# Kernel optimization log

Hardware: AMD Instinct MI355X
Metric: run time of the kernel (lower is better)

The kernel has to match this reference:

```python
import jax, jax.numpy as jnp
import numpy as np

V, E, Hdim, T, B = 32000, 1024, 1024, 64, 32

def setup_inputs() -> dict:
    key = jax.random.key(0)
    ks = jax.random.split(key, 8)
    return {
        "input_x": jax.random.randint(ks[0], (B, T), 0, V, dtype=jnp.int64),
        "initial_state": jnp.zeros((B, Hdim), dtype=jnp.float32),
        "emb": jax.random.normal(ks[1], (V, E), dtype=jnp.float32) * 0.02,
        "H": jax.random.normal(ks[2], (Hdim, Hdim), dtype=jnp.float32) * 0.02,
        "I": jax.random.normal(ks[3], (E, Hdim), dtype=jnp.float32) * 0.02,
        "b1": jax.random.normal(ks[4], (1, Hdim), dtype=jnp.float32) * 0.02,
        "U": jax.random.normal(ks[5], (Hdim, V), dtype=jnp.float32) * 0.02,
        "b2": jax.random.normal(ks[6], (1, V), dtype=jnp.float32) * 0.02,
    }

def reference(input_x, initial_state, emb, H, I, b1, U, b2):
    # Embedding lookup: [B,T] -> [T,B,E] (scan over time)
    x = emb[input_x]                      # [B,T,E]
    x = jnp.transpose(x, (1, 0, 2))       # [T,B,E]

    def step(h, x_t):
        h = jax.nn.sigmoid(h @ H + x_t @ I + b1)  # Elman cell
        return h, h

    final_state, hs = jax.lax.scan(step, initial_state, x)  # hs: [T,B,Hdim]
    # Projection to vocab logits (dropout is identity at eval / p=0)
    logits = jnp.einsum('tbh,hv->tbv', hs, U) + b2          # [T,B,V]
    return logits, final_state
```

## Files before the change

kernel.cpp:

```cpp
#include <hip/hip_runtime.h>


typedef _Float16 f16;
typedef f16 f16x4 __attribute__((ext_vector_type(4)));
typedef f16 f16x8 __attribute__((ext_vector_type(8)));
typedef float f32x4 __attribute__((ext_vector_type(4)));

static constexpr int Vv = 32000, Ee = 1024, Hd = 1024, Tt = 64, Bb = 32;
static constexpr int Mm = Tt * Bb;
static constexpr int NBR = 64;
static constexpr int NBT = 192;

#define GLOAD16(g, l)                                                          \
  __builtin_amdgcn_global_load_lds(                                            \
      (const __attribute__((address_space(1))) void*)(g),                      \
      (__attribute__((address_space(3))) void*)(l), 16, 0, 0)

__global__ __launch_bounds__(256) void prep_all(
    const float* __restrict__ Im, f16* __restrict__ It,
    const float* __restrict__ Hm, f16* __restrict__ Ht,
    const int* __restrict__ tok, const float* __restrict__ emb,
    f16* __restrict__ xg,
    const float* __restrict__ h0, f16* __restrict__ h0f) {
  __shared__ float t[32][33];
  const int tid = threadIdx.x;
  const int bid = blockIdx.x;

  if (bid < 2048) {
    const float* in = (bid < 1024) ? Im : Hm;
    f16* out = (bid < 1024) ? It : Ht;
    const int tile = bid & 1023;
    const int n0 = (tile & 31) * 32, k0 = (tile >> 5) * 32;
    const int tx = tid & 31, ty = tid >> 5;
#pragma unroll
    for (int i = 0; i < 32; i += 8)
      t[ty + i][tx] = in[(size_t)(k0 + ty + i) * 1024 + n0 + tx];
    __syncthreads();
#pragma unroll
    for (int i = 0; i < 32; i += 8)
      out[(size_t)(n0 + ty + i) * 1024 + k0 + tx] = (f16)t[tx][ty + i];
  } else if (bid < 4096) {
    const int m = bid - 2048;
    const int b = m % Bb, tt2 = m / Bb;
    const int token = tok[b * Tt + tt2];
    const float* src = emb + (size_t)token * Ee;
    f16* dst = xg + (size_t)m * Ee;
    const int e = tid * 4;
    float4 v = *(const float4*)(src + e);
    f16x4 o = {(f16)v.x, (f16)v.y, (f16)v.z, (f16)v.w};
    *(f16x4*)(dst + e) = o;
  } else {
    const int i = (bid - 4096) * 256 + tid;
    h0f[i] = (f16)h0[i];
  }
}

__global__ __launch_bounds__(256) void gemm_f16(
    const f16* __restrict__ A, const f16* __restrict__ Bt,
    const float* __restrict__ bias, float* __restrict__ C, int M, int N, int K) {
  __shared__ __align__(16) f16 As[128 * 64];
  __shared__ __align__(16) f16 Bs[128 * 64];

  const int nwg = gridDim.x, bid = blockIdx.x;
  const int cpx = nwg >> 3;
  const int i = (bid & 7) * cpx + (bid >> 3);
  const int ntm = M >> 7;
  const int tm = i % ntm, tn = i / ntm;

  const int tid = threadIdx.x;
  const int lane = tid & 63, wid = tid >> 6;
  const int wm = wid >> 1, wn = wid & 1;

  const int srow = lane >> 3;
  const int sslot = (lane & 7) ^ srow;
  const f16* gA = A + (size_t)(tm * 128 + wid * 8 + srow) * K + sslot * 8;
  const f16* gB = Bt + (size_t)(tn * 128 + wid * 8 + srow) * K + sslot * 8;
  f16* lA = As + wid * 512;
  f16* lB = Bs + wid * 512;

  f32x4 acc[4][4] = {};
  const int r = lane & 15, kb = lane >> 4;

  for (int kc = 0; kc < K; kc += 64) {
    __syncthreads();
#pragma unroll
    for (int rr = 0; rr < 4; ++rr) {
      GLOAD16(gA + (size_t)rr * 32 * K + kc, lA + rr * 2048);
      GLOAD16(gB + (size_t)rr * 32 * K + kc, lB + rr * 2048);
    }
    __syncthreads();

#pragma unroll
    for (int kk = 0; kk < 2; ++kk) {
      f16x8 af[4], bf[4];
#pragma unroll
      for (int ii = 0; ii < 4; ++ii) {
        const int rowA = wm * 64 + ii * 16 + r;
        const int rowB = wn * 64 + ii * 16 + r;
        const int slot = ((kk * 4 + kb) ^ (r & 7)) * 8;
        af[ii] = *(const f16x8*)(As + rowA * 64 + slot);
        bf[ii] = *(const f16x8*)(Bs + rowB * 64 + slot);
      }
#pragma unroll
      for (int ii = 0; ii < 4; ++ii)
#pragma unroll
        for (int jj = 0; jj < 4; ++jj)
          acc[ii][jj] = __builtin_amdgcn_mfma_f32_16x16x32_f16(af[ii], bf[jj], acc[ii][jj], 0, 0, 0);
    }
  }

  const int col0 = tn * 128 + wn * 64, row0 = tm * 128 + wm * 64;
#pragma unroll
  for (int ii = 0; ii < 4; ++ii)
#pragma unroll
    for (int jj = 0; jj < 4; ++jj) {
      int c = col0 + jj * 16 + (lane & 15);
      int rbase = row0 + ii * 16 + (lane >> 4) * 4;
      float bv = bias ? bias[c] : 0.f;
#pragma unroll
      for (int rr = 0; rr < 4; ++rr)
        C[(size_t)(rbase + rr) * N + c] = acc[ii][jj][rr] + bv;
    }
}

#define BAR __builtin_amdgcn_s_barrier()
#define LG0 asm volatile("s_waitcnt lgkmcnt(0)")

__global__ __launch_bounds__(512) void gemm256(
    const f16* __restrict__ A, const f16* __restrict__ Bt,
    const float* __restrict__ bias, float* __restrict__ C,
    int M, int N, int K) {
  __shared__ __align__(16) f16 sm[65536];

  const int nwg = gridDim.x, bid = blockIdx.x;
  const int cpx = nwg >> 3;
  const int ii = (bid & 7) * cpx + (bid >> 3);
  const int ntm = M >> 8;
  const int tm = ii % ntm, tn = ii / ntm;

  const int tid = threadIdx.x;
  const int lane = tid & 63, w = tid >> 6;
  const int wm = w >> 2, wn = w & 3;
  const int r = lane & 15, kb = lane >> 4;

  const int srow = tid >> 3;
  const int slot8 = ((tid & 7) ^ (srow & 7)) * 8;
  const f16* gA = A + (size_t)(tm * 256 + srow) * K + slot8;
  const f16* gB = Bt + (size_t)(tn * 256 + srow) * K + slot8;
  const int lw = w * 512;

  const int NK = K >> 6;

  f32x4 acc[8][4] = {};
  f16x8 a[4][2], b[4][2];

#define STG(kt, ab, R0)                                                        \
  do {                                                                         \
    const f16* gsrc = (ab) ? gB : gA;                                          \
    f16* lb = sm + ((kt) & 1) * 32768 + (ab) * 16384 + (R0) * 64 + lw;         \
    GLOAD16(gsrc + (size_t)(R0) * K + (kt) * 64, lb);                          \
    GLOAD16(gsrc + (size_t)((R0) + 64) * K + (kt) * 64, lb + 4096);            \
  } while (0)

#define LDA(MH)                                                                \
  _Pragma("unroll") for (int i = 0; i < 4; ++i)                                \
  _Pragma("unroll") for (int kk = 0; kk < 2; ++kk)                             \
      a[i][kk] = *(const f16x8*)(Abuf + (wm * 128 + (MH) * 64 + i * 16 + r) * 64 + \
                                 (((kk * 4 + kb) ^ (r & 7)) * 8));

#define LDB(J0)                                                                \
  _Pragma("unroll") for (int j = 0; j < 2; ++j)                                \
  _Pragma("unroll") for (int kk = 0; kk < 2; ++kk)                             \
      b[(J0) + j][kk] = *(const f16x8*)(Bbuf + (wn * 64 + ((J0) + j) * 16 + r) * 64 + \
                                        (((kk * 4 + kb) ^ (r & 7)) * 8));

#define MFMA_Q(MI0, J0)                                                        \
  __builtin_amdgcn_s_setprio(1);                                               \
  _Pragma("unroll") for (int mi = 0; mi < 4; ++mi)                             \
  _Pragma("unroll") for (int j = 0; j < 2; ++j)                                \
  _Pragma("unroll") for (int kk = 0; kk < 2; ++kk)                             \
      acc[(MI0) + mi][(J0) + j] = __builtin_amdgcn_mfma_f32_16x16x32_f16(      \
          a[mi][kk], b[(J0) + j][kk], acc[(MI0) + mi][(J0) + j], 0, 0, 0);     \
  __builtin_amdgcn_s_setprio(0);

  STG(0, 0, 0); STG(0, 0, 128);
  STG(0, 1, 0); STG(0, 1, 128);
  STG(1, 0, 0); STG(1, 0, 128);
  asm volatile("s_waitcnt vmcnt(4)");
  BAR;

  for (int k = 0; k < NK; ++k) {
    const f16* Abuf = sm + (k & 1) * 32768;
    const f16* Bbuf = Abuf + 16384;
    const int kn1 = (k + 1 == NK) ? 0 : k + 1;
    const int kn2 = (k + 2 >= NK) ? k + 2 - NK : k + 2;

    LDA(0); LDB(0);
    STG(kn1, 1, 0);
    BAR; LG0;
    MFMA_Q(0, 0);
    BAR;

    LDB(2);
    STG(kn1, 1, 128);
    BAR; LG0;
    MFMA_Q(0, 2);
    BAR;

    LDA(1);
    BAR; LG0;
    MFMA_Q(4, 2);
    BAR;

    STG(kn2, 0, 0); STG(kn2, 0, 128);
    BAR;
    MFMA_Q(4, 0);
    asm volatile("s_waitcnt vmcnt(4)");
    BAR;
  }

#pragma unroll
  for (int mi = 0; mi < 8; ++mi)
#pragma unroll
    for (int j = 0; j < 4; ++j) {
      int c = tn * 256 + wn * 64 + j * 16 + r;
      int rbase = tm * 256 + wm * 128 + mi * 16 + kb * 4;
      float bv = bias[c];
#pragma unroll
      for (int q = 0; q < 4; ++q)
        __builtin_nontemporal_store(acc[mi][j][q] + bv,
                                    C + (size_t)(rbase + q) * N + c);
    }
#undef STG
#undef LDA
#undef LDB
#undef MFMA_Q
}

__global__ __launch_bounds__(256) void rec_plus_transpose(
    const f16* __restrict__ Ht,
    const float* __restrict__ xI,
    const f16* __restrict__ h0f,
    f16* __restrict__ hs,
    float* __restrict__ hN,
    int* __restrict__ cnt,
    const float* __restrict__ Um,
    f16* __restrict__ Ut) {
  __shared__ float red[4][512];
  __shared__ float tt[32][33];
  const int tid = threadIdx.x;

  if (blockIdx.x >= NBR) {
    const int tb = blockIdx.x - NBR;
    const int tx = tid & 31, ty = tid >> 5;
    const int ntile_n = Vv / 32;
    const int ntiles = ntile_n * (Hd / 32);
    for (int tile = tb; tile < ntiles; tile += NBT) {
      const int n0 = (tile % ntile_n) * 32, k0 = (tile / ntile_n) * 32;
#pragma unroll
      for (int i = 0; i < 32; i += 8)
        tt[ty + i][tx] =
            __builtin_nontemporal_load(Um + (size_t)(k0 + ty + i) * Vv + n0 + tx);
      __syncthreads();
#pragma unroll
      for (int i = 0; i < 32; i += 8)
        Ut[(size_t)(n0 + ty + i) * Hd + k0 + tx] = (f16)tt[tx][ty + i];
      __syncthreads();
      __builtin_amdgcn_s_sleep(16);
    }
    return;
  }

  const int lane = tid & 63, w = tid >> 6;
  const int bn = blockIdx.x;
  const int r = lane & 15, kb = lane >> 4;
  const int colg = bn * 16 + r;

  f16x8 bH[8];
#pragma unroll
  for (int ks = 0; ks < 8; ++ks)
    bH[ks] = *(const f16x8*)(Ht + (size_t)colg * Hd + w * 256 + ks * 32 + kb * 8);

  const int eb = tid >> 3, ecp = tid & 7;

  for (int t = 0; t < Tt; ++t) {
    const f16* hp = t ? hs + (size_t)(t - 1) * Bb * Hd : h0f;
    const float2 xv = *(const float2*)(xI + (size_t)(t * Bb + eb) * Hd + bn * 16 + 2 * ecp);
    f32x4 acc[2] = {};
#pragma unroll
    for (int mt = 0; mt < 2; ++mt) {
      f16x8 af[8];
#pragma unroll
      for (int ks = 0; ks < 8; ++ks)
        af[ks] = *(const f16x8*)(hp + (size_t)(mt * 16 + r) * Hd + w * 256 + ks * 32 + kb * 8);
#pragma unroll
      for (int ks = 0; ks < 8; ++ks)
        acc[mt] = __builtin_amdgcn_mfma_f32_16x16x32_f16(af[ks], bH[ks], acc[mt], 0, 0, 0);
    }
#pragma unroll
    for (int mt = 0; mt < 2; ++mt)
#pragma unroll
      for (int q = 0; q < 4; ++q)
        red[w][mt * 256 + (kb * 4 + q) * 16 + r] = acc[mt][q];
    __syncthreads();

    {
      const float2 r0 = *(const float2*)&red[0][eb * 16 + 2 * ecp];
      const float2 r1 = *(const float2*)&red[1][eb * 16 + 2 * ecp];
      const float2 r2 = *(const float2*)&red[2][eb * 16 + 2 * ecp];
      const float2 r3 = *(const float2*)&red[3][eb * 16 + 2 * ecp];
      float v0 = r0.x + r1.x + r2.x + r3.x + xv.x;
      float v1 = r0.y + r1.y + r2.y + r3.y + xv.y;
      float s0 = 1.f / (1.f + __expf(-v0));
      float s1 = 1.f / (1.f + __expf(-v1));
      union { f16 h[2]; unsigned u; } pk;
      pk.h[0] = (f16)s0;
      pk.h[1] = (f16)s1;
      unsigned* dst = (unsigned*)(hs + (size_t)(t * Bb + eb) * Hd + bn * 16 + 2 * ecp);
      __hip_atomic_store(dst, pk.u, __ATOMIC_RELAXED, __HIP_MEMORY_SCOPE_AGENT);
      if (t == Tt - 1)
        *(float2*)(hN + (size_t)eb * Hd + bn * 16 + 2 * ecp) = make_float2(s0, s1);
    }

    __syncthreads();
    if (tid == 0)
      (void)__hip_atomic_fetch_add(cnt, 1, __ATOMIC_RELAXED, __HIP_MEMORY_SCOPE_AGENT);
    const int target = (t + 1) * NBR;
    while (__hip_atomic_load(cnt, __ATOMIC_RELAXED, __HIP_MEMORY_SCOPE_AGENT) < target)
      __builtin_amdgcn_s_sleep(1);
    asm volatile("" ::: "memory");
  }
}

extern "C" void kernel_launch(void* const* d_in, const int* in_sizes, int n_in,
                              void* d_out, int out_size, void* d_ws, size_t ws_size,
                              hipStream_t stream) {
  const int* input_x = (const int*)d_in[0];
  const float* h0 = (const float*)d_in[1];
  const float* emb = (const float*)d_in[2];
  const float* Hm = (const float*)d_in[3];
  const float* Im = (const float*)d_in[4];
  const float* b1 = (const float*)d_in[5];
  const float* Um = (const float*)d_in[6];
  const float* b2 = (const float*)d_in[7];
  float* out = (float*)d_out;

  char* ws = (char*)d_ws;
  size_t off = 0;
  auto alloc = [&](size_t bytes) { void* p = ws + off; off = (off + bytes + 255) & ~(size_t)255; return p; };
  f16* Ut = (f16*)alloc((size_t)Vv * Hd * 2);
  f16* It = (f16*)alloc((size_t)Hd * Ee * 2);
  f16* Ht = (f16*)alloc((size_t)Hd * Hd * 2);
  f16* xg = (f16*)alloc((size_t)Mm * Ee * 2);
  float* xI = (float*)alloc((size_t)Mm * Hd * 4);
  f16* hs = (f16*)alloc((size_t)Mm * Hd * 2);
  f16* h0f = (f16*)alloc((size_t)Bb * Hd * 2);
  int* cnt = (int*)alloc(256);
  (void)ws_size; (void)in_sizes; (void)n_in; (void)out_size;

  hipMemsetAsync(cnt, 0, sizeof(int), stream);

  prep_all<<<4224, 256, 0, stream>>>(Im, It, Hm, Ht, input_x, emb, xg, h0, h0f);

  gemm_f16<<<(Mm / 128) * (Hd / 128), 256, 0, stream>>>(xg, It, b1, xI, Mm, Hd, Ee);

  rec_plus_transpose<<<NBR + NBT, 256, 0, stream>>>(
      Ht, xI, h0f, hs, out + (size_t)Mm * Vv, cnt, Um, Ut);

  gemm256<<<(Mm / 256) * (Vv / 256), 512, 0, stream>>>(hs, Ut, b2, out, Mm, Vv, Hd);
}
```

Baseline: 459.7 us.

## Fuse recurrence with vocab projection via persistent workers gated on timestep counter

```diff
diff --git a/kernel.cpp b/kernel.cpp
--- a/kernel.cpp
+++ b/kernel.cpp
@@ -9,7 +9,8 @@
 static constexpr int Vv = 32000, Ee = 1024, Hd = 1024, Tt = 64, Bb = 32;
 static constexpr int Mm = Tt * Bb;
 static constexpr int NBR = 64;
-static constexpr int NBT = 192;
+static constexpr int NBW = 192;
+static constexpr int NTM = Mm / 256, NTN = Vv / 256;
 
 #define GLOAD16(g, l)                                                          \
   __builtin_amdgcn_global_load_lds(                                            \
@@ -55,6 +56,20 @@
   }
 }
 
+__global__ void transpose_cvt(const float* __restrict__ in, f16* __restrict__ out,
+                              int K, int N) {
+  __shared__ float t[32][33];
+  int n0 = blockIdx.x * 32, k0 = blockIdx.y * 32;
+  int tx = threadIdx.x, ty = threadIdx.y;
+#pragma unroll
+  for (int i = 0; i < 32; i += 8)
+    t[ty + i][tx] = in[(size_t)(k0 + ty + i) * N + n0 + tx];
+  __syncthreads();
+#pragma unroll
+  for (int i = 0; i < 32; i += 8)
+    out[(size_t)(n0 + ty + i) * K + k0 + tx] = (f16)t[tx][ty + i];
+}
+
 __global__ __launch_bounds__(256) void gemm_f16(
     const f16* __restrict__ A, const f16* __restrict__ Bt,
     const float* __restrict__ bias, float* __restrict__ C, int M, int N, int K) {
@@ -126,40 +141,111 @@
 #define BAR __builtin_amdgcn_s_barrier()
 #define LG0 asm volatile("s_waitcnt lgkmcnt(0)")
 
-__global__ __launch_bounds__(512) void gemm256(
-    const f16* __restrict__ A, const f16* __restrict__ Bt,
-    const float* __restrict__ bias, float* __restrict__ C,
-    int M, int N, int K) {
+__global__ __launch_bounds__(512) void rec_proj(
+    const f16* __restrict__ Ht,
+    const float* __restrict__ xI,
+    const f16* __restrict__ h0f,
+    f16* __restrict__ hs,
+    float* __restrict__ hN,
+    int* __restrict__ cnt,
+    const f16* __restrict__ Ut,
+    const float* __restrict__ b2,
+    float* __restrict__ out) {
   __shared__ __align__(16) f16 sm[65536];
-
-  const int nwg = gridDim.x, bid = blockIdx.x;
-  const int cpx = nwg >> 3;
-  const int ii = (bid & 7) * cpx + (bid >> 3);
-  const int ntm = M >> 8;
-  const int tm = ii % ntm, tn = ii / ntm;
-
   const int tid = threadIdx.x;
-  const int lane = tid & 63, w = tid >> 6;
-  const int wm = w >> 2, wn = w & 3;
-  const int r = lane & 15, kb = lane >> 4;
-
-  const int srow = tid >> 3;
-  const int slot8 = ((tid & 7) ^ (srow & 7)) * 8;
-  const f16* gA = A + (size_t)(tm * 256 + srow) * K + slot8;
-  const f16* gB = Bt + (size_t)(tn * 256 + srow) * K + slot8;
-  const int lw = w * 512;
-
-  const int NK = K >> 6;
-
-  f32x4 acc[8][4] = {};
-  f16x8 a[4][2], b[4][2];
+  const int bid = blockIdx.x;
+
+  if (bid < NBR) {
+    float(*red)[512] = (float(*)[512])sm;
+    const int lane = tid & 63, w = tid >> 6;
+    const bool act = tid < 256;
+    const int bn = bid;
+    const int r = lane & 15, kb = lane >> 4;
+    const int colg = bn * 16 + r;
+
+    f16x8 bH[8];
+    if (act) {
+#pragma unroll
+      for (int ks = 0; ks < 8; ++ks)
+        bH[ks] = *(const f16x8*)(Ht + (size_t)colg * Hd + w * 256 + ks * 32 + kb * 8);
+    }
+    const int eb = tid >> 3, ecp = tid & 7;
+
+    for (int t = 0; t < Tt; ++t) {
+      if (act) {
+        const f16* hp = t ? hs + (size_t)(t - 1) * Bb * Hd : h0f;
+        const float2 xv = *(const float2*)(xI + (size_t)(t * Bb + eb) * Hd + bn * 16 + 2 * ecp);
+        f32x4 acc[2] = {};
+#pragma unroll
+        for (int mt = 0; mt < 2; ++mt) {
+          f16x8 af[8];
+#pragma unroll
+          for (int ks = 0; ks < 8; ++ks)
+            af[ks] = *(const f16x8*)(hp + (size_t)(mt * 16 + r) * Hd + w * 256 + ks * 32 + kb * 8);
+#pragma unroll
+          for (int ks = 0; ks < 8; ++ks)
+            acc[mt] = __builtin_amdgcn_mfma_f32_16x16x32_f16(af[ks], bH[ks], acc[mt], 0, 0, 0);
+        }
+#pragma unroll
+        for (int mt = 0; mt < 2; ++mt)
+#pragma unroll
+          for (int q = 0; q < 4; ++q)
+            red[w][mt * 256 + (kb * 4 + q) * 16 + r] = acc[mt][q];
+        __syncthreads();
+        const float2 r0 = *(const float2*)&red[0][eb * 16 + 2 * ecp];
+        const float2 r1 = *(const float2*)&red[1][eb * 16 + 2 * ecp];
+        const float2 r2 = *(const float2*)&red[2][eb * 16 + 2 * ecp];
+        const float2 r3 = *(const float2*)&red[3][eb * 16 + 2 * ecp];
+        float v0 = r0.x + r1.x + r2.x + r3.x + xv.x;
+        float v1 = r0.y + r1.y + r2.y + r3.y + xv.y;
+        float s0 = 1.f / (1.f + __expf(-v0));
+        float s1 = 1.f / (1.f + __expf(-v1));
+        union { f16 h[2]; unsigned u; } pk;
+        pk.h[0] = (f16)s0;
+        pk.h[1] = (f16)s1;
+        unsigned* dst = (unsigned*)(hs + (size_t)(t * Bb + eb) * Hd + bn * 16 + 2 * ecp);
+        __hip_atomic_store(dst, pk.u, __ATOMIC_RELAXED, __HIP_MEMORY_SCOPE_AGENT);
+        if (t == Tt - 1)
+          *(float2*)(hN + (size_t)eb * Hd + bn * 16 + 2 * ecp) = make_float2(s0, s1);
+      } else {
+        __syncthreads();
+      }
+
+      __syncthreads();
+      if (tid == 0)
+        (void)__hip_atomic_fetch_add(cnt, 1, __ATOMIC_RELAXED, __HIP_MEMORY_SCOPE_AGENT);
+      const int target = (t + 1) * NBR;
+      while (__hip_atomic_load(cnt, __ATOMIC_RELAXED, __HIP_MEMORY_SCOPE_AGENT) < target)
+        __builtin_amdgcn_s_sleep(1);
+      asm volatile("" ::: "memory");
+    }
+  } else {
+    const int wkr = bid - NBR;
+    const int lane = tid & 63, w = tid >> 6;
+    const int wm = w >> 2, wn = w & 3;
+    const int r = lane & 15, kb = lane >> 4;
+    const int srow = tid >> 3;
+    const int slot8 = ((tid & 7) ^ (srow & 7)) * 8;
+    const int lw = w * 512;
+
+    for (int idx = wkr; idx < NTM * NTN; idx += NBW) {
+      const int tm = idx / NTN, tn = idx % NTN;
+      const int tgt = NBR * 8 * (tm + 1);
+      while (__hip_atomic_load(cnt, __ATOMIC_RELAXED, __HIP_MEMORY_SCOPE_AGENT) < tgt)
+        __builtin_amdgcn_s_sleep(32);
+      asm volatile("" ::: "memory");
+
+      const f16* gA = hs + (size_t)(tm * 256 + srow) * Hd + slot8;
+      const f16* gB = Ut + (size_t)(tn * 256 + srow) * Hd + slot8;
+      f32x4 acc[8][4] = {};
+      f16x8 a[4][2], b[4][2];
 
 #define STG(kt, ab, R0)                                                        \
   do {                                                                         \
     const f16* gsrc = (ab) ? gB : gA;                                          \
     f16* lb = sm + ((kt) & 1) * 32768 + (ab) * 16384 + (R0) * 64 + lw;         \
-    GLOAD16(gsrc + (size_t)(R0) * K + (kt) * 64, lb);                          \
-    GLOAD16(gsrc + (size_t)((R0) + 64) * K + (kt) * 64, lb + 4096);            \
+    GLOAD16(gsrc + (size_t)(R0) * Hd + (kt) * 64, lb);                         \
+    GLOAD16(gsrc + (size_t)((R0) + 64) * Hd + (kt) * 64, lb + 4096);           \
   } while (0)
 
 #define LDA(MH)                                                                \
@@ -183,152 +269,60 @@
           a[mi][kk], b[(J0) + j][kk], acc[(MI0) + mi][(J0) + j], 0, 0, 0);     \
   __builtin_amdgcn_s_setprio(0);
 
-  STG(0, 0, 0); STG(0, 0, 128);
-  STG(0, 1, 0); STG(0, 1, 128);
-  STG(1, 0, 0); STG(1, 0, 128);
-  asm volatile("s_waitcnt vmcnt(4)");
-  BAR;
-
-  for (int k = 0; k < NK; ++k) {
-    const f16* Abuf = sm + (k & 1) * 32768;
-    const f16* Bbuf = Abuf + 16384;
-    const int kn1 = (k + 1 == NK) ? 0 : k + 1;
-    const int kn2 = (k + 2 >= NK) ? k + 2 - NK : k + 2;
-
-    LDA(0); LDB(0);
-    STG(kn1, 1, 0);
-    BAR; LG0;
-    MFMA_Q(0, 0);
-    BAR;
-
-    LDB(2);
-    STG(kn1, 1, 128);
-    BAR; LG0;
-    MFMA_Q(0, 2);
-    BAR;
-
-    LDA(1);
-    BAR; LG0;
-    MFMA_Q(4, 2);
-    BAR;
-
-    STG(kn2, 0, 0); STG(kn2, 0, 128);
-    BAR;
-    MFMA_Q(4, 0);
-    asm volatile("s_waitcnt vmcnt(4)");
-    BAR;
-  }
-
-#pragma unroll
-  for (int mi = 0; mi < 8; ++mi)
-#pragma unroll
-    for (int j = 0; j < 4; ++j) {
-      int c = tn * 256 + wn * 64 + j * 16 + r;
-      int rbase = tm * 256 + wm * 128 + mi * 16 + kb * 4;
-      float bv = bias[c];
-#pragma unroll
-      for (int q = 0; q < 4; ++q)
-        __builtin_nontemporal_store(acc[mi][j][q] + bv,
-                                    C + (size_t)(rbase + q) * N + c);
-    }
+      STG(0, 0, 0); STG(0, 0, 128);
+      STG(0, 1, 0); STG(0, 1, 128);
+      STG(1, 0, 0); STG(1, 0, 128);
+      asm volatile("s_waitcnt vmcnt(4)");
+      BAR;
+
+      const int NK = Hd >> 6;
+      for (int k = 0; k < NK; ++k) {
+        const f16* Abuf = sm + (k & 1) * 32768;
+        const f16* Bbuf = Abuf + 16384;
+        const int kn1 = (k + 1 == NK) ? 0 : k + 1;
+        const int kn2 = (k + 2 >= NK) ? k + 2 - NK : k + 2;
+
+        LDA(0); LDB(0);
+        STG(kn1, 1, 0);
+        BAR; LG0;
+        MFMA_Q(0, 0);
+        BAR;
+
+        LDB(2);
+        STG(kn1, 1, 128);
+        BAR; LG0;
+        MFMA_Q(0, 2);
+        BAR;
+
+        LDA(1);
+        BAR; LG0;
+        MFMA_Q(4, 2);
+        BAR;
+
+        STG(kn2, 0, 0); STG(kn2, 0, 128);
+        BAR;
+        MFMA_Q(4, 0);
+        asm volatile("s_waitcnt vmcnt(4)");
+        BAR;
+      }
+
+#pragma unroll
+      for (int mi = 0; mi < 8; ++mi)
+#pragma unroll
+        for (int j = 0; j < 4; ++j) {
+          int c = tn * 256 + wn * 64 + j * 16 + r;
+          int rbase = tm * 256 + wm * 128 + mi * 16 + kb * 4;
+          float bv = b2[c];
+#pragma unroll
+          for (int q = 0; q < 4; ++q)
+            __builtin_nontemporal_store(acc[mi][j][q] + bv,
+                                        out + (size_t)(rbase + q) * Vv + c);
+        }
 #undef STG
 #undef LDA
 #undef LDB
 #undef MFMA_Q
-}
-
-__global__ __launch_bounds__(256) void rec_plus_transpose(
-    const f16* __restrict__ Ht,
-    const float* __restrict__ xI,
-    const f16* __restrict__ h0f,
-    f16* __restrict__ hs,
-    float* __restrict__ hN,
-    int* __restrict__ cnt,
-    const float* __restrict__ Um,
-    f16* __restrict__ Ut) {
-  __shared__ float red[4][512];
-  __shared__ float tt[32][33];
-  const int tid = threadIdx.x;
-
-  if (blockIdx.x >= NBR) {
-    const int tb = blockIdx.x - NBR;
-    const int tx = tid & 31, ty = tid >> 5;
-    const int ntile_n = Vv / 32;
-    const int ntiles = ntile_n * (Hd / 32);
-    for (int tile = tb; tile < ntiles; tile += NBT) {
-      const int n0 = (tile % ntile_n) * 32, k0 = (tile / ntile_n) * 32;
-#pragma unroll
-      for (int i = 0; i < 32; i += 8)
-        tt[ty + i][tx] =
-            __builtin_nontemporal_load(Um + (size_t)(k0 + ty + i) * Vv + n0 + tx);
-      __syncthreads();
-#pragma unroll
-      for (int i = 0; i < 32; i += 8)
-        Ut[(size_t)(n0 + ty + i) * Hd + k0 + tx] = (f16)tt[tx][ty + i];
-      __syncthreads();
-      __builtin_amdgcn_s_sleep(16);
-    }
-    return;
-  }
-
-  const int lane = tid & 63, w = tid >> 6;
-  const int bn = blockIdx.x;
-  const int r = lane & 15, kb = lane >> 4;
-  const int colg = bn * 16 + r;
-
-  f16x8 bH[8];
-#pragma unroll
-  for (int ks = 0; ks < 8; ++ks)
-    bH[ks] = *(const f16x8*)(Ht + (size_t)colg * Hd + w * 256 + ks * 32 + kb * 8);
-
-  const int eb = tid >> 3, ecp = tid & 7;
-
-  for (int t = 0; t < Tt; ++t) {
-    const f16* hp = t ? hs + (size_t)(t - 1) * Bb * Hd : h0f;
-    const float2 xv = *(const float2*)(xI + (size_t)(t * Bb + eb) * Hd + bn * 16 + 2 * ecp);
-    f32x4 acc[2] = {};
-#pragma unroll
-    for (int mt = 0; mt < 2; ++mt) {
-      f16x8 af[8];
-#pragma unroll
-      for (int ks = 0; ks < 8; ++ks)
-        af[ks] = *(const f16x8*)(hp + (size_t)(mt * 16 + r) * Hd + w * 256 + ks * 32 + kb * 8);
-#pragma unroll
-      for (int ks = 0; ks < 8; ++ks)
-        acc[mt] = __builtin_amdgcn_mfma_f32_16x16x32_f16(af[ks], bH[ks], acc[mt], 0, 0, 0);
-    }
-#pragma unroll
-    for (int mt = 0; mt < 2; ++mt)
-#pragma unroll
-      for (int q = 0; q < 4; ++q)
-        red[w][mt * 256 + (kb * 4 + q) * 16 + r] = acc[mt][q];
-    __syncthreads();
-
-    {
-      const float2 r0 = *(const float2*)&red[0][eb * 16 + 2 * ecp];
-      const float2 r1 = *(const float2*)&red[1][eb * 16 + 2 * ecp];
-      const float2 r2 = *(const float2*)&red[2][eb * 16 + 2 * ecp];
-      const float2 r3 = *(const float2*)&red[3][eb * 16 + 2 * ecp];
-      float v0 = r0.x + r1.x + r2.x + r3.x + xv.x;
-      float v1 = r0.y + r1.y + r2.y + r3.y + xv.y;
-      float s0 = 1.f / (1.f + __expf(-v0));
-      float s1 = 1.f / (1.f + __expf(-v1));
-      union { f16 h[2]; unsigned u; } pk;
-      pk.h[0] = (f16)s0;
-      pk.h[1] = (f16)s1;
-      unsigned* dst = (unsigned*)(hs + (size_t)(t * Bb + eb) * Hd + bn * 16 + 2 * ecp);
-      __hip_atomic_store(dst, pk.u, __ATOMIC_RELAXED, __HIP_MEMORY_SCOPE_AGENT);
-      if (t == Tt - 1)
-        *(float2*)(hN + (size_t)eb * Hd + bn * 16 + 2 * ecp) = make_float2(s0, s1);
-    }
-
-    __syncthreads();
-    if (tid == 0)
-      (void)__hip_atomic_fetch_add(cnt, 1, __ATOMIC_RELAXED, __HIP_MEMORY_SCOPE_AGENT);
-    const int target = (t + 1) * NBR;
-    while (__hip_atomic_load(cnt, __ATOMIC_RELAXED, __HIP_MEMORY_SCOPE_AGENT) < target)
-      __builtin_amdgcn_s_sleep(1);
-    asm volatile("" ::: "memory");
+    }
   }
 }
 
@@ -362,10 +356,10 @@
 
   prep_all<<<4224, 256, 0, stream>>>(Im, It, Hm, Ht, input_x, emb, xg, h0, h0f);
 
+  transpose_cvt<<<dim3(Vv / 32, Hd / 32), dim3(32, 8), 0, stream>>>(Um, Ut, Hd, Vv);
+
   gemm_f16<<<(Mm / 128) * (Hd / 128), 256, 0, stream>>>(xg, It, b1, xI, Mm, Hd, Ee);
 
-  rec_plus_transpose<<<NBR + NBT, 256, 0, stream>>>(
-      Ht, xI, h0f, hs, out + (size_t)Mm * Vv, cnt, Um, Ut);
-
-  gemm256<<<(Mm / 256) * (Vv / 256), 512, 0, stream>>>(hs, Ut, b2, out, Mm, Vv, Hd);
-}
+  rec_proj<<<NBR + NBW, 512, 0, stream>>>(
+      Ht, xI, h0f, hs, out + (size_t)Mm * Vv, cnt, Ut, b2, out);
+}
```

After: 511.0 us. 1.11x slower.
